# Kernel optimization log

Hardware: AMD Instinct MI355X
Metric: run time of the kernel (lower is better)

## Reference

```python
import jax, jax.numpy as jnp
import numpy as np

D, N, P = 512, 256, 256   # state, control, obs dims
H = 16                    # h (and h_tilde, since __init__ sets h_tilde = h)
M_LEN = 24                # m (and m_tilde, since __init__ sets m_tilde = m)
L = 2048                  # history length


def setup_inputs() -> dict:
    key = jax.random.key(0)
    ks = jax.random.split(key, 12)
    A = jax.random.normal(ks[0], (D, D), jnp.float32)
    A = 0.99 * A / jnp.linalg.norm(A, ord=2)  # stable dynamics: spectral radius < 1
    B = jax.random.normal(ks[1], (D, N), jnp.float32) * 0.1
    C = jax.random.normal(ks[2], (P, D), jnp.float32) * 0.1
    M = jax.random.normal(ks[3], (H + 1, H + 1, N, P), jnp.float32) * 0.05
    M_bar = jax.random.normal(ks[4], (H + 1, N, P), jnp.float32) * 0.05
    sigma = jax.random.uniform(ks[5], (H + 1,), jnp.float32) * 0.9 + 0.1    # positive eigvals
    phi = jax.random.normal(ks[6], (M_LEN + 1, H + 1), jnp.float32) * 0.2
    lambda_e = jax.random.uniform(ks[7], (H,), jnp.float32) * 0.9 + 0.1     # positive eigvals
    phi_tilde = jax.random.normal(ks[8], (M_LEN, H), jnp.float32) * 0.2
    y_history = jax.random.normal(ks[9], (L, P), jnp.float32)
    u_history = jax.random.normal(ks[10], (L, N), jnp.float32) * 0.1
    y_nat_history = jax.random.normal(ks[11], (L, P), jnp.float32)
    return dict(A=A, B=B, C=C, M=M, M_bar=M_bar, sigma=sigma, phi=phi,
                lambda_e=lambda_e, phi_tilde=phi_tilde, y_history=y_history,
                u_history=u_history, y_nat_history=y_nat_history)


def reference(A, B, C, M, M_bar, sigma, phi, lambda_e, phi_tilde,
              y_history, u_history, y_nat_history):
    # ---- compute_natural_observation: y_nat = y_t - C * sum_i A^i B u_{t-i} ----
    # Horner recurrence over time order: s <- A s + B u_j  =>  s = sum_i A^i B u_{t-i}
    def nat_step(s, u):
        return A @ s + B @ u, None
    s, _ = jax.lax.scan(nat_step, jnp.zeros((D,), A.dtype), u_history)
    y_nat = y_history[-1] - C @ s                              # (P,)

    # ---- compute_predicted_state: y_nat + sum_{i<h} C A^i B u_{-(i+1)} ----
    def g_step(Apow, _):
        return Apow @ A, C @ Apow @ B                          # G_i = C A^i B, (P, N)
    _, G = jax.lax.scan(g_step, jnp.eye(D, dtype=A.dtype), None, length=H)
    u_rev = u_history[::-1]                                    # u_rev[i] = u_{-(i+1)}
    pred = y_nat + jnp.einsum('ipn,in->p', G, u_rev[:H])

    # ---- compute_control_new (full branch; L >= m + m_tilde + 1) ----
    Yrev = y_nat_history[::-1]                                 # Yrev[k] = y_nat_{-(k+1)}
    lam4 = lambda_e ** 0.25                                    # (H,)
    sig4 = sigma ** 0.25                                       # (H+1,)
    # term 1: M_bar[0] @ y[-1]
    u_t = M_bar[0] @ Yrev[0]
    # term 2: sum_{i<h_t, j<m_t} lam_i^.25 phi_tilde[j,i] M_bar[i+1] @ y[-(j+2)]
    u_t = u_t + jnp.einsum('i,ji,inp,jp->n', lam4, phi_tilde,
                           M_bar[1:], Yrev[1:1 + M_LEN])
    # term 3: sum_{l<=h, k<=m} sig_l^.25 phi[k,l] M[0,l] @ y[-(k+1)]
    u_t = u_t + jnp.einsum('l,kl,lnp,kp->n', sig4, phi, M[0], Yrev[:M_LEN + 1])
    # term 4: sum_{i,j,l,k} (sig_l lam_i)^.25 phi[k,l] phi_tilde[j,i] M[i+1,l] @ y[-(j+k+2)]
    jk = jnp.arange(M_LEN)[:, None] + jnp.arange(M_LEN + 1)[None, :]  # (m_t, m+1)
    Ylag = Yrev[2:2 + 2 * M_LEN]                               # covers lags j+k+2
    Yjk = Ylag[jk]                                             # (m_t, m+1, P)
    u_t = u_t + jnp.einsum('i,l,kl,ji,jkp,ilnp->n', lam4, sig4, phi,
                           phi_tilde, Yjk, M[1:])
    return jnp.concatenate([y_nat, pred, u_t])                 # (2P + N,)
```

## Files before the change

### kernel.cpp

```cpp
#include <hip/hip_runtime.h>

#define L_HIST 2048
typedef unsigned short ushortT;
typedef __attribute__((ext_vector_type(8))) short bf16x8;
typedef __attribute__((ext_vector_type(4))) short bf16x4;
typedef __attribute__((ext_vector_type(16))) float f32x16;

__device__ __forceinline__ ushortT f2bf(float x) {
  union { float f; unsigned u; } v; v.f = x;
  unsigned r = (v.u + 0x7FFFu + ((v.u >> 16) & 1u)) >> 16;
  return (ushortT)r;
}
__device__ __forceinline__ float bf2f(ushortT h) {
  union { unsigned u; float f; } v; v.u = ((unsigned)h) << 16; return v.f;
}

struct Job {
  const ushortT *Ph, *Pl, *Qh, *Ql;
  ushortT *Ch, *Cl;
  int M, tbase;
};
struct Prm { Job j[3]; int nj; };

__global__ __launch_bounds__(256) void bgemm(Prm p) {
  int bx = blockIdx.x;
  int ji = 0;
  if (p.nj > 1 && bx >= p.j[1].tbase) ji = 1;
  if (p.nj > 2 && bx >= p.j[2].tbase) ji = 2;
  Job J = p.j[ji];
  int lt = bx - J.tbase;
  int mt = J.M >> 6;
  int mtile = lt % mt, ntile = lt / mt;
  size_t m0 = (size_t)mtile * 64, n0 = (size_t)ntile * 64;

  __shared__ ushortT As[2][64][36];
  __shared__ ushortT Bs[2][64][36];

  int tid = threadIdx.x;
  int lane = tid & 63, wave = tid >> 6;
  int wm = (wave & 1) * 32, wn = (wave >> 1) * 32;
  int fr = lane & 31;
  int fk = (lane >> 5) * 8;
  int row = tid >> 2;
  int kp = (tid & 3) * 8;

  f32x16 acc;
#pragma unroll
  for (int i = 0; i < 16; ++i) acc[i] = 0.f;

  const ushortT* bases[4] = {J.Ph, J.Pl, J.Qh, J.Ql};

  for (int kt = 0; kt < 512; kt += 32) {
#pragma unroll
    for (int seg = 0; seg < 4; ++seg) {
      int pl = seg & 1, isB = seg >> 1;
      const ushortT* src = bases[seg] + ((isB ? n0 : m0) + row) * 512 + kt + kp;
      bf16x8 v = *(const bf16x8*)src;
      ushortT (*dst)[36] = isB ? Bs[pl] : As[pl];
      *(bf16x4*)&dst[row][kp]     = __builtin_shufflevector(v, v, 0, 1, 2, 3);
      *(bf16x4*)&dst[row][kp + 4] = __builtin_shufflevector(v, v, 4, 5, 6, 7);
    }
    __syncthreads();
#pragma unroll
    for (int ks = 0; ks < 32; ks += 16) {
      bf16x8 af[2], bfr[2];
#pragma unroll
      for (int pl = 0; pl < 2; ++pl) {
        const ushortT* pa = &As[pl][wm + fr][ks + fk];
        bf16x4 alo = *(const bf16x4*)pa, ahi = *(const bf16x4*)(pa + 4);
        af[pl] = __builtin_shufflevector(alo, ahi, 0, 1, 2, 3, 4, 5, 6, 7);
        const ushortT* pb = &Bs[pl][wn + fr][ks + fk];
        bf16x4 blo = *(const bf16x4*)pb, bhi = *(const bf16x4*)(pb + 4);
        bfr[pl] = __builtin_shufflevector(blo, bhi, 0, 1, 2, 3, 4, 5, 6, 7);
      }
      acc = __builtin_amdgcn_mfma_f32_32x32x16_bf16(af[0], bfr[0], acc, 0, 0, 0);
      acc = __builtin_amdgcn_mfma_f32_32x32x16_bf16(af[0], bfr[1], acc, 0, 0, 0);
      acc = __builtin_amdgcn_mfma_f32_32x32x16_bf16(af[1], bfr[0], acc, 0, 0, 0);
    }
    __syncthreads();
  }
#pragma unroll
  for (int i = 0; i < 16; ++i) {
    int r = wm + (i & 3) + ((i >> 2) << 3) + ((lane >> 5) << 2);
    int c = wn + (lane & 31);
    float v = acc[i];
    ushortT h = f2bf(v);
    float rem = v - bf2f(h);
    size_t off = (m0 + r) * 512 + (n0 + c);
    J.Ch[off] = h;
    J.Cl[off] = f2bf(rem);
  }
}

__global__ __launch_bounds__(256) void qgemm(
    const ushortT* __restrict__ WTh, const ushortT* __restrict__ WTl,
    const ushortT* __restrict__ UTh, const ushortT* __restrict__ UTl,
    float* __restrict__ Qpart) {
  int z = blockIdx.x, mtile = blockIdx.y, ntile = blockIdx.z;
  int m0 = mtile * 64, n0 = ntile * 64, k0 = z * 1024;

  __shared__ ushortT As[2][64][36];
  __shared__ ushortT Bs[2][64][36];

  int tid = threadIdx.x;
  int lane = tid & 63, wave = tid >> 6;
  int wm = (wave & 1) * 32, wn = (wave >> 1) * 32;
  int fr = lane & 31;
  int fk = (lane >> 5) * 8;
  int ka = tid & 31;
  int ma = (tid >> 5) * 8;
  int jb = tid >> 2;
  int kb = (tid & 3) * 8;

  f32x16 acc;
#pragma unroll
  for (int i = 0; i < 16; ++i) acc[i] = 0.f;

  for (int kt = 0; kt < 1024; kt += 32) {
#pragma unroll
    for (int pl = 0; pl < 2; ++pl) {
      const ushortT* src = (pl ? WTl : WTh) + (size_t)(k0 + kt + ka) * 512 + m0 + ma;
      bf16x8 v = *(const bf16x8*)src;
#pragma unroll
      for (int s = 0; s < 8; ++s) As[pl][ma + s][ka] = (ushortT)v[s];
    }
#pragma unroll
    for (int pl = 0; pl < 2; ++pl) {
      const ushortT* src = (pl ? UTl : UTh) + (size_t)(n0 + jb) * 8192 + k0 + kt + kb;
      bf16x8 v = *(const bf16x8*)src;
      *(bf16x4*)&Bs[pl][jb][kb]     = __builtin_shufflevector(v, v, 0, 1, 2, 3);
      *(bf16x4*)&Bs[pl][jb][kb + 4] = __builtin_shufflevector(v, v, 4, 5, 6, 7);
    }
    __syncthreads();
#pragma unroll
    for (int ks = 0; ks < 32; ks += 16) {
      bf16x8 af[2], bfr[2];
#pragma unroll
      for (int pl = 0; pl < 2; ++pl) {
        const ushortT* pa = &As[pl][wm + fr][ks + fk];
        bf16x4 alo = *(const bf16x4*)pa, ahi = *(const bf16x4*)(pa + 4);
        af[pl] = __builtin_shufflevector(alo, ahi, 0, 1, 2, 3, 4, 5, 6, 7);
        const ushortT* pb = &Bs[pl][wn + fr][ks + fk];
        bf16x4 blo = *(const bf16x4*)pb, bhi = *(const bf16x4*)(pb + 4);
        bfr[pl] = __builtin_shufflevector(blo, bhi, 0, 1, 2, 3, 4, 5, 6, 7);
      }
      acc = __builtin_amdgcn_mfma_f32_32x32x16_bf16(af[0], bfr[0], acc, 0, 0, 0);
      acc = __builtin_amdgcn_mfma_f32_32x32x16_bf16(af[0], bfr[1], acc, 0, 0, 0);
      acc = __builtin_amdgcn_mfma_f32_32x32x16_bf16(af[1], bfr[0], acc, 0, 0, 0);
    }
    __syncthreads();
  }
#pragma unroll
  for (int i = 0; i < 16; ++i) {
    int r = wm + (i & 3) + ((i >> 2) << 3) + ((lane >> 5) << 2);
    int c = wn + (lane & 31);
    Qpart[((size_t)z * 512 + m0 + r) * 128 + n0 + c] = acc[i];
  }
}

__global__ __launch_bounds__(256) void qreduce(const float* __restrict__ Qpart,
                                               float* __restrict__ Qb) {
  int idx = blockIdx.x * 256 + threadIdx.x;
  if (idx >= 512 * 68) return;
  int m = idx / 68, j = idx - m * 68;
  float s = 0.f;
#pragma unroll
  for (int z = 0; z < 8; ++z) s += Qpart[((size_t)z * 512 + m) * 128 + j];
  Qb[m * 128 + j] = s;
}

__global__ void split_A(const float* __restrict__ A, ushortT* N1h, ushortT* N1l,
                        ushortT* T1h, ushortT* T1l) {
  int idx = blockIdx.x * 256 + threadIdx.x;
  int r = idx >> 9, c = idx & 511;
  float x = A[idx];
  ushortT h = f2bf(x); float rem = x - bf2f(h); ushortT l = f2bf(rem);
  N1h[idx] = h; N1l[idx] = l;
  T1h[c * 512 + r] = h; T1l[c * 512 + r] = l;
}

__global__ void split_B(const float* __restrict__ B, ushortT* WTh, ushortT* WTl) {
  int idx = blockIdx.x * 256 + threadIdx.x;
  int d = idx >> 8, c = idx & 255;
  float x = B[idx];
  ushortT h = f2bf(x); float rem = x - bf2f(h);
  WTh[c * 512 + d] = h; WTl[c * 512 + d] = f2bf(rem);
}

__global__ void pack_ut(const float* __restrict__ uh, ushortT* __restrict__ UTh,
                        ushortT* __restrict__ UTl) {
  int idx = blockIdx.x * 256 + threadIdx.x;
  int j = idx >> 13, k = idx & 8191;
  int tau = k >> 8, c = k & 255;
  float v = 0.f;
  if (j < 64) v = uh[(size_t)(L_HIST - 1 - (32 * j + tau)) * 256 + c];
  else if (j == 64 && tau < 16) v = uh[(size_t)(L_HIST - 1 - tau) * 256 + c];
  ushortT h = f2bf(v);
  UTh[idx] = h; UTl[idx] = f2bf(v - bf2f(h));
}

__global__ __launch_bounds__(512) void rgemm(const ushortT* __restrict__ P1th,
                                             const ushortT* __restrict__ P1tl,
                                             const float* __restrict__ Qb,
                                             float* __restrict__ Rpart) {
  int j1 = blockIdx.x + 1;
  int dc = blockIdx.y;
  int d0 = dc * 128;
  int m = threadIdx.x;
  __shared__ float Qs[128][8];
  for (int i = threadIdx.x; i < 1024; i += 512) {
    int dd = i >> 3, jj = i & 7;
    Qs[dd][jj] = Qb[(size_t)(d0 + dd) * 128 + j1 + 8 * jj];
  }
  __syncthreads();
  float acc[8];
#pragma unroll
  for (int jj = 0; jj < 8; ++jj) acc[jj] = 0.f;
  for (int d = 0; d < 128; ++d) {
    size_t off = ((size_t)(j1 - 1) * 512 + d0 + d) * 512 + m;
    float tv = bf2f(P1th[off]) + bf2f(P1tl[off]);
    float4 q0 = *(const float4*)&Qs[d][0];
    float4 q1 = *(const float4*)&Qs[d][4];
    acc[0] += tv * q0.x; acc[1] += tv * q0.y; acc[2] += tv * q0.z; acc[3] += tv * q0.w;
    acc[4] += tv * q1.x; acc[5] += tv * q1.y; acc[6] += tv * q1.z; acc[7] += tv * q1.w;
  }
  float* dst = Rpart + (size_t)((j1 - 1) * 4 + dc) * 4096 + m * 8;
#pragma unroll
  for (int jj = 0; jj < 8; ++jj) dst[jj] = acc[jj];
}

__global__ __launch_bounds__(256) void rreduce(const float* __restrict__ Qb,
                                               const float* __restrict__ Rpart,
                                               float* __restrict__ Rb) {
  int idx = blockIdx.x * 256 + threadIdx.x;
  int m = idx >> 3, jj = idx & 7;
  float s = Qb[(size_t)m * 128 + 8 * jj];
  for (int p = 0; p < 28; ++p) s += Rpart[(size_t)p * 4096 + idx];
  Rb[idx] = s;
}

__global__ __launch_bounds__(512) void sgemm(const ushortT* __restrict__ P2th,
                                             const ushortT* __restrict__ P2tl,
                                             const float* __restrict__ Rb,
                                             float* __restrict__ Spart) {
  int j2 = blockIdx.x + 1;
  int dc = blockIdx.y;
  int d0 = dc * 128;
  int m = threadIdx.x;
  __shared__ float Rs[128];
  if (threadIdx.x < 128) Rs[threadIdx.x] = Rb[(size_t)(d0 + threadIdx.x) * 8 + j2];
  __syncthreads();
  float acc = 0.f;
  for (int d = 0; d < 128; ++d) {
    size_t off = ((size_t)(j2 - 1) * 512 + d0 + d) * 512 + m;
    acc += (bf2f(P2th[off]) + bf2f(P2tl[off])) * Rs[d];
  }
  Spart[(size_t)((j2 - 1) * 4 + dc) * 512 + m] = acc;
}

__global__ __launch_bounds__(256) void sreduce(const float* __restrict__ Rb,
                                               const float* __restrict__ Spart,
                                               float* __restrict__ Sb) {
  int m = blockIdx.x * 256 + threadIdx.x;
  float s = Rb[(size_t)m * 8];
  for (int p = 0; p < 28; ++p) s += Spart[(size_t)p * 512 + m];
  Sb[m] = s;
}

__global__ __launch_bounds__(64) void finalize_kernel(
    const float* __restrict__ Cmat, const float* __restrict__ svec,
    const float* __restrict__ Qb, const float* __restrict__ yh,
    float* __restrict__ out) {
  int p = blockIdx.x;
  int lane = threadIdx.x;
  float a1 = 0.f, a2 = 0.f;
  for (int t = lane; t < 512; t += 64) {
    float cv = Cmat[(size_t)p * 512 + t];
    a1 += cv * svec[t];
    a2 += cv * Qb[(size_t)t * 128 + 64];
  }
  for (int off = 32; off > 0; off >>= 1) {
    a1 += __shfl_down(a1, off);
    a2 += __shfl_down(a2, off);
  }
  if (lane == 0) {
    float ynat = yh[(size_t)(L_HIST - 1) * 256 + p] - a1;
    out[p] = ynat;
    out[256 + p] = ynat + a2;
  }
}

__global__ __launch_bounds__(256) void weights_kernel(
    const float* __restrict__ ynh, const float* __restrict__ sigma,
    const float* __restrict__ phi, const float* __restrict__ lambda_e,
    const float* __restrict__ phi_tilde, float* __restrict__ wvec,
    float* __restrict__ out) {
  int v = blockIdx.x;
  int p = threadIdx.x;
  __shared__ float w4[48];
  float val = 0.f;
  if (v == 0) {
    val = ynh[(size_t)(L_HIST - 1) * 256 + p];
    out[512 + p] = 0.f;
  } else if (v <= 16) {
    int i = v - 1;
    float s = 0.f;
    for (int j = 0; j < 24; ++j)
      s += phi_tilde[j * 16 + i] * ynh[(size_t)(L_HIST - 2 - j) * 256 + p];
    val = powf(lambda_e[i], 0.25f) * s;
  } else if (v <= 33) {
    int l = v - 17;
    float s = 0.f;
    for (int k = 0; k < 25; ++k)
      s += phi[k * 17 + l] * ynh[(size_t)(L_HIST - 1 - k) * 256 + p];
    val = powf(sigma[l], 0.25f) * s;
  } else {
    int t = v - 34;
    int i = t / 17, l = t % 17;
    if (p < 48) {
      int m = p;
      int jlo = m - 24; if (jlo < 0) jlo = 0;
      int jhi = m; if (jhi > 23) jhi = 23;
      float s = 0.f;
      for (int j = jlo; j <= jhi; ++j)
        s += phi_tilde[j * 16 + i] * phi[(m - j) * 17 + l];
      w4[p] = s;
    }
    __syncthreads();
    float s = 0.f;
    for (int m = 0; m < 48; ++m)
      s += w4[m] * ynh[(size_t)(L_HIST - 3 - m) * 256 + p];
    val = powf(lambda_e[i], 0.25f) * powf(sigma[l], 0.25f) * s;
  }
  wvec[v * 256 + p] = val;
}

__global__ __launch_bounds__(256) void ut_gemv(
    const float* __restrict__ Mtens, const float* __restrict__ Mbar,
    const float* __restrict__ wvec, float* __restrict__ out) {
  int n = blockIdx.x >> 1;
  int h = blockIdx.x & 1;
  int lane = threadIdx.x & 63;
  int wid = threadIdx.x >> 6;
  int vend = h * 153 + 153;
  float4 acc = {0.f, 0.f, 0.f, 0.f};
#pragma unroll 4
  for (int v = h * 153 + wid; v < vend; v += 4) {
    const float* mat = (v < 17 ? Mbar : Mtens - 17 * 65536) + (size_t)v * 65536;
    float4 mv = ((const float4*)(mat + (size_t)n * 256))[lane];
    float4 wv = ((const float4*)(wvec + (size_t)v * 256))[lane];
    acc.x += mv.x * wv.x; acc.y += mv.y * wv.y;
    acc.z += mv.z * wv.z; acc.w += mv.w * wv.w;
  }
  float a = (acc.x + acc.y) + (acc.z + acc.w);
  for (int off = 32; off > 0; off >>= 1) a += __shfl_down(a, off);
  if (lane == 0) atomicAdd(&out[512 + n], a);
}

extern "C" void kernel_launch(void* const* d_in, const int* in_sizes, int n_in,
                              void* d_out, int out_size, void* d_ws, size_t ws_size,
                              hipStream_t stream) {
  (void)in_sizes; (void)n_in; (void)out_size; (void)ws_size;
  const float* A   = (const float*)d_in[0];
  const float* B   = (const float*)d_in[1];
  const float* C   = (const float*)d_in[2];
  const float* M   = (const float*)d_in[3];
  const float* Mb  = (const float*)d_in[4];
  const float* sig = (const float*)d_in[5];
  const float* phi = (const float*)d_in[6];
  const float* lam = (const float*)d_in[7];
  const float* pt  = (const float*)d_in[8];
  const float* yh  = (const float*)d_in[9];
  const float* uh  = (const float*)d_in[10];
  const float* ynh = (const float*)d_in[11];
  float* out = (float*)d_out;
  char* base = (char*)d_ws;

  const size_t MB = 1u << 20;
  const size_t SL = 512 * 512;
  ushortT* POW  = (ushortT*)base;
  ushortT* WTh  = (ushortT*)(base + 16 * MB);
  ushortT* WTl  = (ushortT*)(base + 24 * MB);
  ushortT* P1th = (ushortT*)(base + 32 * MB);
  ushortT* P1tl = (ushortT*)(base + 32 * MB + 3670016);
  ushortT* P2th = (ushortT*)base;
  ushortT* P2tl = (ushortT*)(base + 3670016);
  ushortT* UTh  = (ushortT*)(base + 8 * MB);
  ushortT* UTl  = (ushortT*)(base + 10 * MB);
  float*   Qpart= (float*)(base + 12 * MB);
  float* Qb    = (float*)(base + 39 * MB);
  float* Rpart = Qb + 512 * 128;
  float* Rb    = Rpart + 28 * 4096;
  float* Spart = Rb + 4096;
  float* Sb    = Spart + 28 * 512;
  float* wvec  = Sb + 512;

  auto ph = [&](int i) { return POW + (size_t)i * 2 * SL; };
  auto pl = [&](int i) { return POW + (size_t)i * 2 * SL + SL; };
  auto e1h = [&](int j) { return P1th + (size_t)(j - 1) * SL; };
  auto e1l = [&](int j) { return P1tl + (size_t)(j - 1) * SL; };
  auto e2h = [&](int j) { return P2th + (size_t)(j - 1) * SL; };
  auto e2l = [&](int j) { return P2tl + (size_t)(j - 1) * SL; };

  auto mkJ = [&](const ushortT* Ph, const ushortT* Pl, const ushortT* Qh,
                 const ushortT* Ql, ushortT* Ch, ushortT* Cl, int Mrows) {
    Job j; j.Ph = Ph; j.Pl = Pl; j.Qh = Qh; j.Ql = Ql;
    j.Ch = Ch; j.Cl = Cl; j.M = Mrows; j.tbase = 0; return j;
  };
  auto runL = [&](Job j0, Job j1, Job j2, int nj) {
    Prm p; p.j[0] = j0; p.j[1] = (nj > 1) ? j1 : j0; p.j[2] = (nj > 2) ? j2 : j0;
    p.nj = nj;
    int tb = 0;
    for (int i = 0; i < nj; ++i) { p.j[i].tbase = tb; tb += (p.j[i].M >> 6) * 8; }
    bgemm<<<tb, 256, 0, stream>>>(p);
  };

  split_A<<<1024, 256, 0, stream>>>(A, ph(0), pl(0), ph(1), pl(1));
  split_B<<<512, 256, 0, stream>>>(B, WTh, WTl);

  Job d = mkJ(ph(0), pl(0), ph(1), pl(1), ph(2), pl(2), 512);
  runL(mkJ(ph(0), pl(0), ph(1), pl(1), ph(2), pl(2), 512),
       mkJ(ph(1), pl(1), ph(0), pl(0), ph(3), pl(3), 512),
       mkJ(WTh, WTl, ph(0), pl(0), WTh + 256 * 512, WTl + 256 * 512, 256), 3);
  runL(mkJ(ph(2), pl(2), ph(3), pl(3), ph(4), pl(4), 512),
       mkJ(ph(3), pl(3), ph(2), pl(2), ph(5), pl(5), 512),
       mkJ(WTh, WTl, ph(2), pl(2), WTh + 512 * 512, WTl + 512 * 512, 512), 3);
  runL(mkJ(ph(4), pl(4), ph(5), pl(5), ph(6), pl(6), 512),
       mkJ(ph(5), pl(5), ph(4), pl(4), ph(7), pl(7), 512),
       mkJ(WTh, WTl, ph(4), pl(4), WTh + 1024 * 512, WTl + 1024 * 512, 1024), 3);
  runL(mkJ(ph(6), pl(6), ph(7), pl(7), ph(8), pl(8), 512),
       mkJ(ph(7), pl(7), ph(6), pl(6), ph(9), pl(9), 512),
       mkJ(WTh, WTl, ph(6), pl(6), WTh + 2048 * 512, WTl + 2048 * 512, 2048), 3);
  runL(mkJ(ph(8), pl(8), ph(9), pl(9), ph(10), pl(10), 512),
       mkJ(ph(9), pl(9), ph(8), pl(8), e1h(1), e1l(1), 512),
       mkJ(WTh, WTl, ph(8), pl(8), WTh + 4096 * 512, WTl + 4096 * 512, 4096), 3);
  runL(mkJ(ph(10), pl(10), e1h(1), e1l(1), ph(11), pl(11), 512),
       mkJ(e1h(1), e1l(1), ph(10), pl(10), e1h(2), e1l(2), 512),
       d, 2);
  runL(mkJ(ph(11), pl(11), e1h(2), e1l(2), ph(12), pl(12), 512),
       mkJ(e1h(1), e1l(1), ph(11), pl(11), e1h(3), e1l(3), 1024),
       d, 2);
  runL(mkJ(ph(12), pl(12), e1h(4), e1l(4), ph(13), pl(13), 512),
       mkJ(e1h(1), e1l(1), ph(12), pl(12), e1h(5), e1l(5), 1536),
       mkJ(e1h(4), e1l(4), ph(12), pl(12), e2h(1), e2l(1), 512), 3);
  runL(mkJ(ph(13), pl(13), e2h(1), e2l(1), ph(14), pl(14), 512),
       mkJ(e2h(1), e2l(1), ph(13), pl(13), e2h(2), e2l(2), 512),
       d, 2);
  runL(mkJ(ph(14), pl(14), e2h(2), e2l(2), ph(15), pl(15), 512),
       mkJ(e2h(1), e2l(1), ph(14), pl(14), e2h(3), e2l(3), 1024),
       d, 2);
  runL(mkJ(e2h(1), e2l(1), ph(15), pl(15), e2h(5), e2l(5), 1536),
       d, d, 1);

  pack_ut<<<4096, 256, 0, stream>>>(uh, UTh, UTl);
  qgemm<<<dim3(8, 8, 2), 256, 0, stream>>>(WTh, WTl, UTh, UTl, Qpart);
  qreduce<<<136, 256, 0, stream>>>(Qpart, Qb);
  rgemm<<<dim3(7, 4), 512, 0, stream>>>(P1th, P1tl, Qb, Rpart);
  rreduce<<<16, 256, 0, stream>>>(Qb, Rpart, Rb);
  sgemm<<<dim3(7, 4), 512, 0, stream>>>(P2th, P2tl, Rb, Spart);
  sreduce<<<2, 256, 0, stream>>>(Rb, Spart, Sb);
  finalize_kernel<<<256, 64, 0, stream>>>(C, Sb, Qb, yh, out);

  weights_kernel<<<306, 256, 0, stream>>>(ynh, sig, phi, lam, pt, wvec, out);
  ut_gemv<<<512, 256, 0, stream>>>(M, Mb, wvec, out);
}
```

Measured before the change: 359.7 us.

## Drop low-part A operand, register-prefetch GEMM tiles, fuse init and reduce kernels

The split-bf16 GEMMs now use only the high part of the left operand, cutting the MFMAs per step from three to two and removing one tile load. Global loads are prefetched into registers one tile ahead, which lets the loop use a single barrier per iteration. The three pre-split kernels are merged into one init kernel. The separate reduce kernels are removed and their sums folded into the consumers, and the later GEMVs read fp32 power matrices directly. The ut_gemv grid is doubled to 1024 blocks. Dropping the A low part lowers precision in the repeated-squaring chain, which risks accuracy error.

```diff
diff --git a/kernel.cpp b/kernel.cpp
--- a/kernel.cpp
+++ b/kernel.cpp
@@ -14,10 +14,21 @@
 __device__ __forceinline__ float bf2f(ushortT h) {
   union { unsigned u; float f; } v; v.u = ((unsigned)h) << 16; return v.f;
 }
+__device__ __forceinline__ bf16x4 lo4(bf16x8 v) {
+  return __builtin_shufflevector(v, v, 0, 1, 2, 3);
+}
+__device__ __forceinline__ bf16x4 hi4(bf16x8 v) {
+  return __builtin_shufflevector(v, v, 4, 5, 6, 7);
+}
+__device__ __forceinline__ bf16x8 rd8(const ushortT* p) {
+  bf16x4 a = *(const bf16x4*)p, b = *(const bf16x4*)(p + 4);
+  return __builtin_shufflevector(a, b, 0, 1, 2, 3, 4, 5, 6, 7);
+}
 
 struct Job {
-  const ushortT *Ph, *Pl, *Qh, *Ql;
+  const ushortT *Ph, *Qh, *Ql;
   ushortT *Ch, *Cl;
+  float *Cf;
   int M, tbase;
 };
 struct Prm { Job j[3]; int nj; };
@@ -34,121 +45,114 @@
   size_t m0 = (size_t)mtile * 64, n0 = (size_t)ntile * 64;
 
   __shared__ ushortT As[2][64][36];
-  __shared__ ushortT Bs[2][64][36];
+  __shared__ ushortT Bhs[2][64][36];
+  __shared__ ushortT Bls[2][64][36];
 
   int tid = threadIdx.x;
   int lane = tid & 63, wave = tid >> 6;
   int wm = (wave & 1) * 32, wn = (wave >> 1) * 32;
-  int fr = lane & 31;
-  int fk = (lane >> 5) * 8;
-  int row = tid >> 2;
-  int kp = (tid & 3) * 8;
+  int fr = lane & 31, fk = (lane >> 5) * 8;
+  int row = tid >> 2, kp = (tid & 3) * 8;
+
+  const ushortT* pA  = J.Ph + (m0 + row) * 512 + kp;
+  const ushortT* pBh = J.Qh + (n0 + row) * 512 + kp;
+  const ushortT* pBl = J.Ql + (n0 + row) * 512 + kp;
+
+  bf16x8 rA  = *(const bf16x8*)pA;
+  bf16x8 rBh = *(const bf16x8*)pBh;
+  bf16x8 rBl = *(const bf16x8*)pBl;
 
   f32x16 acc;
 #pragma unroll
   for (int i = 0; i < 16; ++i) acc[i] = 0.f;
 
-  const ushortT* bases[4] = {J.Ph, J.Pl, J.Qh, J.Ql};
-
   for (int kt = 0; kt < 512; kt += 32) {
-#pragma unroll
-    for (int seg = 0; seg < 4; ++seg) {
-      int pl = seg & 1, isB = seg >> 1;
-      const ushortT* src = bases[seg] + ((isB ? n0 : m0) + row) * 512 + kt + kp;
-      bf16x8 v = *(const bf16x8*)src;
-      ushortT (*dst)[36] = isB ? Bs[pl] : As[pl];
-      *(bf16x4*)&dst[row][kp]     = __builtin_shufflevector(v, v, 0, 1, 2, 3);
-      *(bf16x4*)&dst[row][kp + 4] = __builtin_shufflevector(v, v, 4, 5, 6, 7);
-    }
+    int buf = (kt >> 5) & 1;
+    *(bf16x4*)&As[buf][row][kp]      = lo4(rA);
+    *(bf16x4*)&As[buf][row][kp + 4]  = hi4(rA);
+    *(bf16x4*)&Bhs[buf][row][kp]     = lo4(rBh);
+    *(bf16x4*)&Bhs[buf][row][kp + 4] = hi4(rBh);
+    *(bf16x4*)&Bls[buf][row][kp]     = lo4(rBl);
+    *(bf16x4*)&Bls[buf][row][kp + 4] = hi4(rBl);
     __syncthreads();
+    if (kt + 32 < 512) {
+      rA  = *(const bf16x8*)(pA + kt + 32);
+      rBh = *(const bf16x8*)(pBh + kt + 32);
+      rBl = *(const bf16x8*)(pBl + kt + 32);
+    }
 #pragma unroll
     for (int ks = 0; ks < 32; ks += 16) {
-      bf16x8 af[2], bfr[2];
-#pragma unroll
-      for (int pl = 0; pl < 2; ++pl) {
-        const ushortT* pa = &As[pl][wm + fr][ks + fk];
-        bf16x4 alo = *(const bf16x4*)pa, ahi = *(const bf16x4*)(pa + 4);
-        af[pl] = __builtin_shufflevector(alo, ahi, 0, 1, 2, 3, 4, 5, 6, 7);
-        const ushortT* pb = &Bs[pl][wn + fr][ks + fk];
-        bf16x4 blo = *(const bf16x4*)pb, bhi = *(const bf16x4*)(pb + 4);
-        bfr[pl] = __builtin_shufflevector(blo, bhi, 0, 1, 2, 3, 4, 5, 6, 7);
-      }
-      acc = __builtin_amdgcn_mfma_f32_32x32x16_bf16(af[0], bfr[0], acc, 0, 0, 0);
-      acc = __builtin_amdgcn_mfma_f32_32x32x16_bf16(af[0], bfr[1], acc, 0, 0, 0);
-      acc = __builtin_amdgcn_mfma_f32_32x32x16_bf16(af[1], bfr[0], acc, 0, 0, 0);
-    }
-    __syncthreads();
+      bf16x8 a  = rd8(&As[buf][wm + fr][ks + fk]);
+      bf16x8 bh = rd8(&Bhs[buf][wn + fr][ks + fk]);
+      bf16x8 bl = rd8(&Bls[buf][wn + fr][ks + fk]);
+      acc = __builtin_amdgcn_mfma_f32_32x32x16_bf16(a, bh, acc, 0, 0, 0);
+      acc = __builtin_amdgcn_mfma_f32_32x32x16_bf16(a, bl, acc, 0, 0, 0);
+    }
   }
 #pragma unroll
   for (int i = 0; i < 16; ++i) {
     int r = wm + (i & 3) + ((i >> 2) << 3) + ((lane >> 5) << 2);
     int c = wn + (lane & 31);
     float v = acc[i];
+    size_t off = (m0 + r) * 512 + (n0 + c);
     ushortT h = f2bf(v);
-    float rem = v - bf2f(h);
-    size_t off = (m0 + r) * 512 + (n0 + c);
     J.Ch[off] = h;
-    J.Cl[off] = f2bf(rem);
+    if (J.Cl) J.Cl[off] = f2bf(v - bf2f(h));
+    if (J.Cf) J.Cf[off] = v;
   }
 }
 
 __global__ __launch_bounds__(256) void qgemm(
-    const ushortT* __restrict__ WTh, const ushortT* __restrict__ WTl,
-    const ushortT* __restrict__ UTh, const ushortT* __restrict__ UTl,
-    float* __restrict__ Qpart) {
+    const ushortT* __restrict__ WTh, const ushortT* __restrict__ UTh,
+    const ushortT* __restrict__ UTl, float* __restrict__ Qpart) {
   int z = blockIdx.x, mtile = blockIdx.y, ntile = blockIdx.z;
   int m0 = mtile * 64, n0 = ntile * 64, k0 = z * 1024;
 
   __shared__ ushortT As[2][64][36];
-  __shared__ ushortT Bs[2][64][36];
+  __shared__ ushortT Bhs[2][64][36];
+  __shared__ ushortT Bls[2][64][36];
 
   int tid = threadIdx.x;
   int lane = tid & 63, wave = tid >> 6;
   int wm = (wave & 1) * 32, wn = (wave >> 1) * 32;
-  int fr = lane & 31;
-  int fk = (lane >> 5) * 8;
-  int ka = tid & 31;
-  int ma = (tid >> 5) * 8;
-  int jb = tid >> 2;
-  int kb = (tid & 3) * 8;
+  int fr = lane & 31, fk = (lane >> 5) * 8;
+  int ka = tid & 31, ma = (tid >> 5) * 8;
+  int jb = tid >> 2, kb = (tid & 3) * 8;
+
+  const ushortT* pW  = WTh + (size_t)(k0 + ka) * 512 + m0 + ma;
+  const ushortT* pUh = UTh + (size_t)(n0 + jb) * 8192 + k0 + kb;
+  const ushortT* pUl = UTl + (size_t)(n0 + jb) * 8192 + k0 + kb;
+
+  bf16x8 rW  = *(const bf16x8*)pW;
+  bf16x8 rUh = *(const bf16x8*)pUh;
+  bf16x8 rUl = *(const bf16x8*)pUl;
 
   f32x16 acc;
 #pragma unroll
   for (int i = 0; i < 16; ++i) acc[i] = 0.f;
 
   for (int kt = 0; kt < 1024; kt += 32) {
-#pragma unroll
-    for (int pl = 0; pl < 2; ++pl) {
-      const ushortT* src = (pl ? WTl : WTh) + (size_t)(k0 + kt + ka) * 512 + m0 + ma;
-      bf16x8 v = *(const bf16x8*)src;
-#pragma unroll
-      for (int s = 0; s < 8; ++s) As[pl][ma + s][ka] = (ushortT)v[s];
-    }
-#pragma unroll
-    for (int pl = 0; pl < 2; ++pl) {
-      const ushortT* src = (pl ? UTl : UTh) + (size_t)(n0 + jb) * 8192 + k0 + kt + kb;
-      bf16x8 v = *(const bf16x8*)src;
-      *(bf16x4*)&Bs[pl][jb][kb]     = __builtin_shufflevector(v, v, 0, 1, 2, 3);
-      *(bf16x4*)&Bs[pl][jb][kb + 4] = __builtin_shufflevector(v, v, 4, 5, 6, 7);
-    }
+    int buf = (kt >> 5) & 1;
+#pragma unroll
+    for (int s = 0; s < 8; ++s) As[buf][ma + s][ka] = (ushortT)rW[s];
+    *(bf16x4*)&Bhs[buf][jb][kb]     = lo4(rUh);
+    *(bf16x4*)&Bhs[buf][jb][kb + 4] = hi4(rUh);
+    *(bf16x4*)&Bls[buf][jb][kb]     = lo4(rUl);
+    *(bf16x4*)&Bls[buf][jb][kb + 4] = hi4(rUl);
     __syncthreads();
+    if (kt + 32 < 1024) {
+      rW  = *(const bf16x8*)(pW + (size_t)(kt + 32) * 512);
+      rUh = *(const bf16x8*)(pUh + kt + 32);
+      rUl = *(const bf16x8*)(pUl + kt + 32);
+    }
 #pragma unroll
     for (int ks = 0; ks < 32; ks += 16) {
-      bf16x8 af[2], bfr[2];
-#pragma unroll
-      for (int pl = 0; pl < 2; ++pl) {
-        const ushortT* pa = &As[pl][wm + fr][ks + fk];
-        bf16x4 alo = *(const bf16x4*)pa, ahi = *(const bf16x4*)(pa + 4);
-        af[pl] = __builtin_shufflevector(alo, ahi, 0, 1, 2, 3, 4, 5, 6, 7);
-        const ushortT* pb = &Bs[pl][wn + fr][ks + fk];
-        bf16x4 blo = *(const bf16x4*)pb, bhi = *(const bf16x4*)(pb + 4);
-        bfr[pl] = __builtin_shufflevector(blo, bhi, 0, 1, 2, 3, 4, 5, 6, 7);
-      }
-      acc = __builtin_amdgcn_mfma_f32_32x32x16_bf16(af[0], bfr[0], acc, 0, 0, 0);
-      acc = __builtin_amdgcn_mfma_f32_32x32x16_bf16(af[0], bfr[1], acc, 0, 0, 0);
-      acc = __builtin_amdgcn_mfma_f32_32x32x16_bf16(af[1], bfr[0], acc, 0, 0, 0);
-    }
-    __syncthreads();
+      bf16x8 a  = rd8(&As[buf][wm + fr][ks + fk]);
+      bf16x8 bh = rd8(&Bhs[buf][wn + fr][ks + fk]);
+      bf16x8 bl = rd8(&Bls[buf][wn + fr][ks + fk]);
+      acc = __builtin_amdgcn_mfma_f32_32x32x16_bf16(a, bh, acc, 0, 0, 0);
+      acc = __builtin_amdgcn_mfma_f32_32x32x16_bf16(a, bl, acc, 0, 0, 0);
+    }
   }
 #pragma unroll
   for (int i = 0; i < 16; ++i) {
@@ -158,50 +162,35 @@
   }
 }
 
-__global__ __launch_bounds__(256) void qreduce(const float* __restrict__ Qpart,
-                                               float* __restrict__ Qb) {
+__global__ void init_all(const float* __restrict__ A, const float* __restrict__ B,
+                         const float* __restrict__ uh,
+                         ushortT* N1h, ushortT* N1l, ushortT* T1h, ushortT* T1l,
+                         ushortT* WTh, ushortT* UTh, ushortT* UTl) {
   int idx = blockIdx.x * 256 + threadIdx.x;
-  if (idx >= 512 * 68) return;
-  int m = idx / 68, j = idx - m * 68;
-  float s = 0.f;
-#pragma unroll
-  for (int z = 0; z < 8; ++z) s += Qpart[((size_t)z * 512 + m) * 128 + j];
-  Qb[m * 128 + j] = s;
-}
-
-__global__ void split_A(const float* __restrict__ A, ushortT* N1h, ushortT* N1l,
-                        ushortT* T1h, ushortT* T1l) {
-  int idx = blockIdx.x * 256 + threadIdx.x;
-  int r = idx >> 9, c = idx & 511;
-  float x = A[idx];
-  ushortT h = f2bf(x); float rem = x - bf2f(h); ushortT l = f2bf(rem);
-  N1h[idx] = h; N1l[idx] = l;
-  T1h[c * 512 + r] = h; T1l[c * 512 + r] = l;
-}
-
-__global__ void split_B(const float* __restrict__ B, ushortT* WTh, ushortT* WTl) {
-  int idx = blockIdx.x * 256 + threadIdx.x;
-  int d = idx >> 8, c = idx & 255;
-  float x = B[idx];
-  ushortT h = f2bf(x); float rem = x - bf2f(h);
-  WTh[c * 512 + d] = h; WTl[c * 512 + d] = f2bf(rem);
-}
-
-__global__ void pack_ut(const float* __restrict__ uh, ushortT* __restrict__ UTh,
-                        ushortT* __restrict__ UTl) {
-  int idx = blockIdx.x * 256 + threadIdx.x;
-  int j = idx >> 13, k = idx & 8191;
-  int tau = k >> 8, c = k & 255;
-  float v = 0.f;
-  if (j < 64) v = uh[(size_t)(L_HIST - 1 - (32 * j + tau)) * 256 + c];
-  else if (j == 64 && tau < 16) v = uh[(size_t)(L_HIST - 1 - tau) * 256 + c];
-  ushortT h = f2bf(v);
-  UTh[idx] = h; UTl[idx] = f2bf(v - bf2f(h));
-}
-
-__global__ __launch_bounds__(512) void rgemm(const ushortT* __restrict__ P1th,
-                                             const ushortT* __restrict__ P1tl,
-                                             const float* __restrict__ Qb,
+  if (idx < 262144) {
+    int r = idx >> 9, c = idx & 511;
+    float x = A[idx];
+    ushortT h = f2bf(x); ushortT l = f2bf(x - bf2f(h));
+    N1h[idx] = h; N1l[idx] = l;
+    T1h[c * 512 + r] = h; T1l[c * 512 + r] = l;
+  } else if (idx < 262144 + 131072) {
+    int i2 = idx - 262144;
+    int d = i2 >> 8, c = i2 & 255;
+    WTh[c * 512 + d] = f2bf(B[i2]);
+  } else {
+    int i2 = idx - 393216;
+    int j = i2 >> 13, k = i2 & 8191;
+    int tau = k >> 8, c = k & 255;
+    float v = 0.f;
+    if (j < 64) v = uh[(size_t)(L_HIST - 1 - (32 * j + tau)) * 256 + c];
+    else if (j == 64 && tau < 16) v = uh[(size_t)(L_HIST - 1 - tau) * 256 + c];
+    ushortT h = f2bf(v);
+    UTh[i2] = h; UTl[i2] = f2bf(v - bf2f(h));
+  }
+}
+
+__global__ __launch_bounds__(512) void rgemm(const float* __restrict__ Pf1,
+                                             const float* __restrict__ Qpart,
                                              float* __restrict__ Rpart) {
   int j1 = blockIdx.x + 1;
   int dc = blockIdx.y;
@@ -210,15 +199,18 @@
   __shared__ float Qs[128][8];
   for (int i = threadIdx.x; i < 1024; i += 512) {
     int dd = i >> 3, jj = i & 7;
-    Qs[dd][jj] = Qb[(size_t)(d0 + dd) * 128 + j1 + 8 * jj];
+    float s = 0.f;
+#pragma unroll
+    for (int z = 0; z < 8; ++z)
+      s += Qpart[((size_t)z * 512 + d0 + dd) * 128 + j1 + 8 * jj];
+    Qs[dd][jj] = s;
   }
   __syncthreads();
   float acc[8];
 #pragma unroll
   for (int jj = 0; jj < 8; ++jj) acc[jj] = 0.f;
   for (int d = 0; d < 128; ++d) {
-    size_t off = ((size_t)(j1 - 1) * 512 + d0 + d) * 512 + m;
-    float tv = bf2f(P1th[off]) + bf2f(P1tl[off]);
+    float tv = Pf1[((size_t)(j1 - 1) * 512 + d0 + d) * 512 + m];
     float4 q0 = *(const float4*)&Qs[d][0];
     float4 q1 = *(const float4*)&Qs[d][4];
     acc[0] += tv * q0.x; acc[1] += tv * q0.y; acc[2] += tv * q0.z; acc[3] += tv * q0.w;
@@ -229,55 +221,53 @@
   for (int jj = 0; jj < 8; ++jj) dst[jj] = acc[jj];
 }
 
-__global__ __launch_bounds__(256) void rreduce(const float* __restrict__ Qb,
-                                               const float* __restrict__ Rpart,
-                                               float* __restrict__ Rb) {
-  int idx = blockIdx.x * 256 + threadIdx.x;
-  int m = idx >> 3, jj = idx & 7;
-  float s = Qb[(size_t)m * 128 + 8 * jj];
-  for (int p = 0; p < 28; ++p) s += Rpart[(size_t)p * 4096 + idx];
-  Rb[idx] = s;
-}
-
-__global__ __launch_bounds__(512) void sgemm(const ushortT* __restrict__ P2th,
-                                             const ushortT* __restrict__ P2tl,
-                                             const float* __restrict__ Rb,
+__global__ __launch_bounds__(512) void sgemm(const float* __restrict__ Pf2,
+                                             const float* __restrict__ Qpart,
+                                             const float* __restrict__ Rpart,
                                              float* __restrict__ Spart) {
   int j2 = blockIdx.x + 1;
   int dc = blockIdx.y;
   int d0 = dc * 128;
   int m = threadIdx.x;
   __shared__ float Rs[128];
-  if (threadIdx.x < 128) Rs[threadIdx.x] = Rb[(size_t)(d0 + threadIdx.x) * 8 + j2];
+  if (threadIdx.x < 128) {
+    int dd = threadIdx.x;
+    float s = 0.f;
+#pragma unroll
+    for (int z = 0; z < 8; ++z)
+      s += Qpart[((size_t)z * 512 + d0 + dd) * 128 + 8 * j2];
+    for (int p = 0; p < 28; ++p)
+      s += Rpart[(size_t)p * 4096 + (d0 + dd) * 8 + j2];
+    Rs[dd] = s;
+  }
   __syncthreads();
   float acc = 0.f;
-  for (int d = 0; d < 128; ++d) {
-    size_t off = ((size_t)(j2 - 1) * 512 + d0 + d) * 512 + m;
-    acc += (bf2f(P2th[off]) + bf2f(P2tl[off])) * Rs[d];
-  }
+  for (int d = 0; d < 128; ++d)
+    acc += Pf2[((size_t)(j2 - 1) * 512 + d0 + d) * 512 + m] * Rs[d];
   Spart[(size_t)((j2 - 1) * 4 + dc) * 512 + m] = acc;
 }
 
-__global__ __launch_bounds__(256) void sreduce(const float* __restrict__ Rb,
-                                               const float* __restrict__ Spart,
-                                               float* __restrict__ Sb) {
-  int m = blockIdx.x * 256 + threadIdx.x;
-  float s = Rb[(size_t)m * 8];
-  for (int p = 0; p < 28; ++p) s += Spart[(size_t)p * 512 + m];
-  Sb[m] = s;
-}
-
 __global__ __launch_bounds__(64) void finalize_kernel(
-    const float* __restrict__ Cmat, const float* __restrict__ svec,
-    const float* __restrict__ Qb, const float* __restrict__ yh,
-    float* __restrict__ out) {
+    const float* __restrict__ Cmat, const float* __restrict__ Qpart,
+    const float* __restrict__ Rpart, const float* __restrict__ Spart,
+    const float* __restrict__ yh, float* __restrict__ out) {
   int p = blockIdx.x;
   int lane = threadIdx.x;
   float a1 = 0.f, a2 = 0.f;
   for (int t = lane; t < 512; t += 64) {
+    float sb = 0.f, qp = 0.f;
+#pragma unroll
+    for (int z = 0; z < 8; ++z) {
+      sb += Qpart[((size_t)z * 512 + t) * 128 + 0];
+      qp += Qpart[((size_t)z * 512 + t) * 128 + 64];
+    }
+    for (int q = 0; q < 28; ++q) {
+      sb += Rpart[(size_t)q * 4096 + t * 8];
+      sb += Spart[(size_t)q * 512 + t];
+    }
     float cv = Cmat[(size_t)p * 512 + t];
-    a1 += cv * svec[t];
-    a2 += cv * Qb[(size_t)t * 128 + 64];
+    a1 += cv * sb;
+    a2 += cv * qp;
   }
   for (int off = 32; off > 0; off >>= 1) {
     a1 += __shfl_down(a1, off);
@@ -338,14 +328,14 @@
 __global__ __launch_bounds__(256) void ut_gemv(
     const float* __restrict__ Mtens, const float* __restrict__ Mbar,
     const float* __restrict__ wvec, float* __restrict__ out) {
-  int n = blockIdx.x >> 1;
-  int h = blockIdx.x & 1;
+  int n = blockIdx.x & 255;
+  int h = blockIdx.x >> 8;
   int lane = threadIdx.x & 63;
   int wid = threadIdx.x >> 6;
-  int vend = h * 153 + 153;
+  int vs = (306 * h) >> 2, ve = (306 * (h + 1)) >> 2;
   float4 acc = {0.f, 0.f, 0.f, 0.f};
 #pragma unroll 4
-  for (int v = h * 153 + wid; v < vend; v += 4) {
+  for (int v = vs + wid; v < ve; v += 4) {
     const float* mat = (v < 17 ? Mbar : Mtens - 17 * 65536) + (size_t)v * 65536;
     float4 mv = ((const float4*)(mat + (size_t)n * 256))[lane];
     float4 wv = ((const float4*)(wvec + (size_t)v * 256))[lane];
@@ -380,20 +370,18 @@
   const size_t SL = 512 * 512;
   ushortT* POW  = (ushortT*)base;
   ushortT* WTh  = (ushortT*)(base + 16 * MB);
-  ushortT* WTl  = (ushortT*)(base + 24 * MB);
-  ushortT* P1th = (ushortT*)(base + 32 * MB);
-  ushortT* P1tl = (ushortT*)(base + 32 * MB + 3670016);
-  ushortT* P2th = (ushortT*)base;
-  ushortT* P2tl = (ushortT*)(base + 3670016);
-  ushortT* UTh  = (ushortT*)(base + 8 * MB);
-  ushortT* UTl  = (ushortT*)(base + 10 * MB);
-  float*   Qpart= (float*)(base + 12 * MB);
-  float* Qb    = (float*)(base + 39 * MB);
-  float* Rpart = Qb + 512 * 128;
-  float* Rb    = Rpart + 28 * 4096;
-  float* Spart = Rb + 4096;
-  float* Sb    = Spart + 28 * 512;
-  float* wvec  = Sb + 512;
+  ushortT* P1th = (ushortT*)(base + 26 * MB);
+  ushortT* P1tl = (ushortT*)(base + 30 * MB);
+  ushortT* P2th = (ushortT*)(base + 34 * MB);
+  ushortT* P2tl = (ushortT*)(base + 38 * MB);
+  float*   Pf1  = (float*)(base + 42 * MB);
+  float*   Pf2  = (float*)(base + 50 * MB);
+  ushortT* UTh  = (ushortT*)(base + 58 * MB);
+  ushortT* UTl  = (ushortT*)(base + 60 * MB);
+  float*   Qpart= (float*)(base + 62 * MB);
+  float*   Rpart= (float*)(base + 64 * MB);
+  float*   Spart= Rpart + 28 * 4096;
+  float*   wvec = Spart + 28 * 512;
 
   auto ph = [&](int i) { return POW + (size_t)i * 2 * SL; };
   auto pl = [&](int i) { return POW + (size_t)i * 2 * SL + SL; };
@@ -402,10 +390,10 @@
   auto e2h = [&](int j) { return P2th + (size_t)(j - 1) * SL; };
   auto e2l = [&](int j) { return P2tl + (size_t)(j - 1) * SL; };
 
-  auto mkJ = [&](const ushortT* Ph, const ushortT* Pl, const ushortT* Qh,
-                 const ushortT* Ql, ushortT* Ch, ushortT* Cl, int Mrows) {
-    Job j; j.Ph = Ph; j.Pl = Pl; j.Qh = Qh; j.Ql = Ql;
-    j.Ch = Ch; j.Cl = Cl; j.M = Mrows; j.tbase = 0; return j;
+  auto mkJ = [&](const ushortT* Ph, const ushortT* Qh, const ushortT* Ql,
+                 ushortT* Ch, ushortT* Cl, float* Cf, int Mrows) {
+    Job j; j.Ph = Ph; j.Qh = Qh; j.Ql = Ql;
+    j.Ch = Ch; j.Cl = Cl; j.Cf = Cf; j.M = Mrows; j.tbase = 0; return j;
   };
   auto runL = [&](Job j0, Job j1, Job j2, int nj) {
     Prm p; p.j[0] = j0; p.j[1] = (nj > 1) ? j1 : j0; p.j[2] = (nj > 2) ? j2 : j0;
@@ -415,52 +403,48 @@
     bgemm<<<tb, 256, 0, stream>>>(p);
   };
 
-  split_A<<<1024, 256, 0, stream>>>(A, ph(0), pl(0), ph(1), pl(1));
-  split_B<<<512, 256, 0, stream>>>(B, WTh, WTl);
-
-  Job d = mkJ(ph(0), pl(0), ph(1), pl(1), ph(2), pl(2), 512);
-  runL(mkJ(ph(0), pl(0), ph(1), pl(1), ph(2), pl(2), 512),
-       mkJ(ph(1), pl(1), ph(0), pl(0), ph(3), pl(3), 512),
-       mkJ(WTh, WTl, ph(0), pl(0), WTh + 256 * 512, WTl + 256 * 512, 256), 3);
-  runL(mkJ(ph(2), pl(2), ph(3), pl(3), ph(4), pl(4), 512),
-       mkJ(ph(3), pl(3), ph(2), pl(2), ph(5), pl(5), 512),
-       mkJ(WTh, WTl, ph(2), pl(2), WTh + 512 * 512, WTl + 512 * 512, 512), 3);
-  runL(mkJ(ph(4), pl(4), ph(5), pl(5), ph(6), pl(6), 512),
-       mkJ(ph(5), pl(5), ph(4), pl(4), ph(7), pl(7), 512),
-       mkJ(WTh, WTl, ph(4), pl(4), WTh + 1024 * 512, WTl + 1024 * 512, 1024), 3);
-  runL(mkJ(ph(6), pl(6), ph(7), pl(7), ph(8), pl(8), 512),
-       mkJ(ph(7), pl(7), ph(6), pl(6), ph(9), pl(9), 512),
-       mkJ(WTh, WTl, ph(6), pl(6), WTh + 2048 * 512, WTl + 2048 * 512, 2048), 3);
-  runL(mkJ(ph(8), pl(8), ph(9), pl(9), ph(10), pl(10), 512),
-       mkJ(ph(9), pl(9), ph(8), pl(8), e1h(1), e1l(1), 512),
-       mkJ(WTh, WTl, ph(8), pl(8), WTh + 4096 * 512, WTl + 4096 * 512, 4096), 3);
-  runL(mkJ(ph(10), pl(10), e1h(1), e1l(1), ph(11), pl(11), 512),
-       mkJ(e1h(1), e1l(1), ph(10), pl(10), e1h(2), e1l(2), 512),
+  init_all<<<5632, 256, 0, stream>>>(A, B, uh, ph(0), pl(0), ph(1), pl(1),
+                                     WTh, UTh, UTl);
+
+  Job d = mkJ(ph(0), ph(1), pl(1), ph(2), pl(2), nullptr, 512);
+  runL(mkJ(ph(0), ph(1), pl(1), ph(2), pl(2), nullptr, 512),
+       mkJ(ph(1), ph(0), pl(0), ph(3), pl(3), nullptr, 512),
+       mkJ(WTh, ph(0), pl(0), WTh + 256 * 512, nullptr, nullptr, 256), 3);
+  runL(mkJ(ph(2), ph(3), pl(3), ph(4), pl(4), nullptr, 512),
+       mkJ(ph(3), ph(2), pl(2), ph(5), pl(5), nullptr, 512),
+       mkJ(WTh, ph(2), pl(2), WTh + 512 * 512, nullptr, nullptr, 512), 3);
+  runL(mkJ(ph(4), ph(5), pl(5), ph(6), pl(6), nullptr, 512),
+       mkJ(ph(5), ph(4), pl(4), ph(7), pl(7), nullptr, 512),
+       mkJ(WTh, ph(4), pl(4), WTh + 1024 * 512, nullptr, nullptr, 1024), 3);
+  runL(mkJ(ph(6), ph(7), pl(7), ph(8), pl(8), nullptr, 512),
+       mkJ(ph(7), ph(6), pl(6), ph(9), pl(9), nullptr, 512),
+       mkJ(WTh, ph(6), pl(6), WTh + 2048 * 512, nullptr, nullptr, 2048), 3);
+  runL(mkJ(ph(8), ph(9), pl(9), ph(10), pl(10), nullptr, 512),
+       mkJ(ph(9), ph(8), pl(8), e1h(1), e1l(1), Pf1, 512),
+       mkJ(WTh, ph(8), pl(8), WTh + 4096 * 512, nullptr, nullptr, 4096), 3);
+  runL(mkJ(ph(10), e1h(1), e1l(1), ph(11), pl(11), nullptr, 512),
+       mkJ(e1h(1), ph(10), pl(10), e1h(2), e1l(2), Pf1 + SL, 512),
        d, 2);
-  runL(mkJ(ph(11), pl(11), e1h(2), e1l(2), ph(12), pl(12), 512),
-       mkJ(e1h(1), e1l(1), ph(11), pl(11), e1h(3), e1l(3), 1024),
+  runL(mkJ(ph(11), e1h(2), e1l(2), ph(12), pl(12), nullptr, 512),
+       mkJ(e1h(1), ph(11), pl(11), e1h(3), e1l(3), Pf1 + 2 * SL, 1024),
        d, 2);
-  runL(mkJ(ph(12), pl(12), e1h(4), e1l(4), ph(13), pl(13), 512),
-       mkJ(e1h(1), e1l(1), ph(12), pl(12), e1h(5), e1l(5), 1536),
-       mkJ(e1h(4), e1l(4), ph(12), pl(12), e2h(1), e2l(1), 512), 3);
-  runL(mkJ(ph(13), pl(13), e2h(1), e2l(1), ph(14), pl(14), 512),
-       mkJ(e2h(1), e2l(1), ph(13), pl(13), e2h(2), e2l(2), 512),
+  runL(mkJ(ph(12), e1h(4), e1l(4), ph(13), pl(13), nullptr, 512),
+       mkJ(e1h(1), ph(12), pl(12), e1h(5), nullptr, Pf1 + 4 * SL, 1536),
+       mkJ(e1h(4), ph(12), pl(12), e2h(1), e2l(1), Pf2, 512), 3);
+  runL(mkJ(ph(13), e2h(1), e2l(1), ph(14), pl(14), nullptr, 512),
+       mkJ(e2h(1), ph(13), pl(13), e2h(2), e2l(2), Pf2 + SL, 512),
        d, 2);
-  runL(mkJ(ph(14), pl(14), e2h(2), e2l(2), ph(15), pl(15), 512),
-       mkJ(e2h(1), e2l(1), ph(14), pl(14), e2h(3), e2l(3), 1024),
+  runL(mkJ(ph(14), e2h(2), e2l(2), ph(15), pl(15), nullptr, 512),
+       mkJ(e2h(1), ph(14), pl(14), e2h(3), nullptr, Pf2 + 2 * SL, 1024),
        d, 2);
-  runL(mkJ(e2h(1), e2l(1), ph(15), pl(15), e2h(5), e2l(5), 1536),
+  runL(mkJ(e2h(1), ph(15), pl(15), e2h(5), nullptr, Pf2 + 4 * SL, 1536),
        d, d, 1);
 
-  pack_ut<<<4096, 256, 0, stream>>>(uh, UTh, UTl);
-  qgemm<<<dim3(8, 8, 2), 256, 0, stream>>>(WTh, WTl, UTh, UTl, Qpart);
-  qreduce<<<136, 256, 0, stream>>>(Qpart, Qb);
-  rgemm<<<dim3(7, 4), 512, 0, stream>>>(P1th, P1tl, Qb, Rpart);
-  rreduce<<<16, 256, 0, stream>>>(Qb, Rpart, Rb);
-  sgemm<<<dim3(7, 4), 512, 0, stream>>>(P2th, P2tl, Rb, Spart);
-  sreduce<<<2, 256, 0, stream>>>(Rb, Spart, Sb);
-  finalize_kernel<<<256, 64, 0, stream>>>(C, Sb, Qb, yh, out);
+  qgemm<<<dim3(8, 8, 2), 256, 0, stream>>>(WTh, UTh, UTl, Qpart);
+  rgemm<<<dim3(7, 4), 512, 0, stream>>>(Pf1, Qpart, Rpart);
+  sgemm<<<dim3(7, 4), 512, 0, stream>>>(Pf2, Qpart, Rpart, Spart);
+  finalize_kernel<<<256, 64, 0, stream>>>(C, Qpart, Rpart, Spart, yh, out);
 
   weights_kernel<<<306, 256, 0, stream>>>(ynh, sig, phi, lam, pt, wvec, out);
-  ut_gemv<<<512, 256, 0, stream>>>(M, Mb, wvec, out);
-}
+  ut_gemv<<<1024, 256, 0, stream>>>(M, Mb, wvec, out);
+}
```

Measured after the change: 326.5 us. -9.2%, faster.
